# Kernel tuning notes

Measured on AMD Instinct MI355X. Metric: run time of the kernel, lower is better.

## Reference

```python
import jax, jax.numpy as jnp
import numpy as np
from jax import lax

# dims: B=2, C=dim=64, H=W=128 -> N=16384 tokens; d_inner=128, d_state=16, dt_rank=4, d_conv=4

def setup_inputs() -> dict:
    key = jax.random.key(0)
    ks = jax.random.split(key, 8)
    def n(k, shp, scale=0.02):
        return jax.random.normal(k, shp, jnp.float32) * scale
    d_inner, d_state, dt_rank = 128, 16, 4
    return {
        "x": jax.random.normal(ks[0], (2, 64, 128, 128), jnp.float32),
        "ln_w": jnp.ones((64,), jnp.float32),
        "ln_b": jnp.zeros((64,), jnp.float32),
        "in_proj_w": n(ks[1], (2 * d_inner, 64)),
        "conv_w": n(ks[2], (d_inner, 1, 4), 0.1),
        "conv_b": jnp.zeros((d_inner,), jnp.float32),
        "x_proj_w": n(ks[3], (dt_rank + 2 * d_state, d_inner)),
        "dt_proj_w": n(ks[4], (d_inner, dt_rank), 0.5),
        "dt_proj_b": n(ks[5], (d_inner,), 0.1),
        "A_log": jnp.log(jnp.broadcast_to(jnp.arange(1, d_state + 1, dtype=jnp.float32), (d_inner, d_state))),
        "D_param": jnp.ones((d_inner,), jnp.float32),
        "out_proj_w": n(ks[6], (64, d_inner)),
        "out_proj_b": jnp.zeros((64,), jnp.float32),
    }


def reference(x, ln_w, ln_b, in_proj_w, conv_w, conv_b, x_proj_w,
              dt_proj_w, dt_proj_b, A_log, D_param, out_proj_w, out_proj_b):
    B, C, H, W = x.shape
    d_inner = in_proj_w.shape[0] // 2
    d_state = A_log.shape[1]
    dt_rank = dt_proj_w.shape[1]
    eps = 1e-5

    # feature2token + channel LayerNorm (Restormer WithBias LN over C)
    t = x.reshape(B, C, H * W).transpose(0, 2, 1)  # [B, N, C]
    mu = jnp.mean(t, axis=-1, keepdims=True)
    var = jnp.var(t, axis=-1, keepdims=True)
    t = (t - mu) * lax.rsqrt(var + eps) * ln_w + ln_b

    # in_proj -> x, z
    xz = jnp.einsum('bnc,dc->bnd', t, in_proj_w)  # [B, N, 2*d_inner]
    x_in, z = jnp.split(xz, 2, axis=-1)

    # depthwise causal conv1d (k=4, pad left 3), then SiLU
    u = lax.conv_general_dilated(
        x_in.transpose(0, 2, 1), conv_w,
        window_strides=(1,), padding=[(3, 0)],
        feature_group_count=d_inner,
        dimension_numbers=('NCH', 'OIH', 'NCH'))
    u = jax.nn.silu(u + conv_b[None, :, None]).transpose(0, 2, 1)  # [B, N, d_inner]

    # x_proj -> dt, B, C of the SSM
    x_dbl = jnp.einsum('bnd,ed->bne', u, x_proj_w)
    dt_r = x_dbl[..., :dt_rank]
    Bmat = x_dbl[..., dt_rank:dt_rank + d_state]   # [B, N, d_state]
    Cmat = x_dbl[..., dt_rank + d_state:]          # [B, N, d_state]
    dt = jax.nn.softplus(jnp.einsum('bnr,dr->bnd', dt_r, dt_proj_w) + dt_proj_b)

    # selective scan: h_t = exp(dt*A) h_{t-1} + dt*B*u
    A = -jnp.exp(A_log)  # [d_inner, d_state]
    deltaA = jnp.exp(jnp.einsum('bnd,ds->bnds', dt, A))
    deltaBu = jnp.einsum('bnd,bns,bnd->bnds', dt, Bmat, u)

    def combine(c1, c2):
        a1, b1 = c1
        a2, b2 = c2
        return a2 * a1, a2 * b1 + b2

    _, h = lax.associative_scan(combine, (deltaA, deltaBu), axis=1)  # h: [B, N, d_inner, d_state]

    y = jnp.einsum('bnds,bns->bnd', h, Cmat) + u * D_param
    y = y * jax.nn.silu(z)
    out = jnp.einsum('bnd,cd->bnc', y, out_proj_w) + out_proj_b  # [B, N, C]

    # token2feature
    return out.transpose(0, 2, 1).reshape(B, C, H, W)
```

## Files before the change

### kernel.cpp

```cpp
#include <hip/hip_runtime.h>
#include <math.h>

#define NTOK 16384
#define DIN  128
#define NCH  512
#define CHL  32
#define NG   32
#define GCH  16

__device__ __forceinline__ float silu_f(float x)    { return x / (1.f + __expf(-x)); }
__device__ __forceinline__ float softplus_f(float x){ return (x > 20.f) ? x : log1pf(__expf(x)); }

__global__ __launch_bounds__(256) void k12(
    const float* __restrict__ x, const float* __restrict__ lnw,
    const float* __restrict__ lnb, const float* __restrict__ Win,
    const float* __restrict__ cw, const float* __restrict__ cb,
    float* __restrict__ zbuf, float* __restrict__ u)
{
  __shared__ __align__(16) float bufA[128*69];
  __shared__ __align__(16) float bufB[67*68];
  __shared__ float ps[256], pq[256];
  __shared__ float mu[67], rs[67];

  int t = threadIdx.x;
  int b  = blockIdx.x >> 8;
  int n0 = (blockIdx.x & 255) << 6;
  const float* xb = x + (size_t)b*64*NTOK;

  int tok = t & 63, quad = t >> 6;
  float s0 = 0.f, s1 = 0.f;
  for (int i = 0; i < 16; ++i) {
    int c = i*4 + quad;
    float v = xb[(size_t)c*NTOK + n0 + tok];
    bufA[c*68 + tok + 3] = v;
    s0 += v; s1 += v*v;
  }
  ps[t] = s0; pq[t] = s1;
  float vh = 0.f;
  if (t < 192) {
    int c = t & 63, k = t >> 6;
    int n = n0 - 3 + k;
    vh = (n >= 0) ? xb[(size_t)c*NTOK + n] : 0.f;
    bufA[c*68 + k] = vh;
  }
  __syncthreads();
  if (t < 192) {
    float a0 = vh, a1 = vh*vh;
    #pragma unroll
    for (int m = 1; m < 64; m <<= 1) { a0 += __shfl_xor(a0, m); a1 += __shfl_xor(a1, m); }
    if ((t & 63) == 0) {
      int k = t >> 6;
      float m = a0 * 0.015625f;
      float q = a1 * 0.015625f - m*m;
      mu[k] = m; rs[k] = rsqrtf(q + 1e-5f);
    }
  }
  if (t < 64) {
    float m = ps[t] + ps[64+t] + ps[128+t] + ps[192+t];
    float q = pq[t] + pq[64+t] + pq[128+t] + pq[192+t];
    m *= 0.015625f;
    q = q*0.015625f - m*m;
    mu[t+3] = m; rs[t+3] = rsqrtf(q + 1e-5f);
  }
  __syncthreads();
  {
    int c = t & 63, tq = t >> 6;
    float wv = lnw[c], bv = lnb[c];
    #pragma unroll
    for (int i = 0; i < 17; ++i) {
      int tp = tq + 4*i;
      if (tp < 67) {
        float val = (tp < 3 && n0 == 0) ? 0.f
                  : (bufA[c*68 + tp] - mu[tp]) * rs[tp] * wv + bv;
        bufB[tp*68 + c] = val;
      }
    }
  }

  int tokg = t & 15, dg = t >> 4;
  const float4* TB = (const float4*)bufB;

  __syncthreads();
  for (int i = 0; i < 32; ++i) {
    int idx = i*256 + t;
    int c = idx & 63, dd = idx >> 6;
    bufA[dd*68 + c] = Win[(128 + dd)*64 + c];
  }
  __syncthreads();
  {
    const float4* WA = (const float4*)bufA;
    float acc[4][8];
    #pragma unroll
    for (int i = 0; i < 4; ++i)
      #pragma unroll
      for (int j = 0; j < 8; ++j) acc[i][j] = 0.f;
    #pragma unroll 4
    for (int c4 = 0; c4 < 16; ++c4) {
      float4 tv[4], wv[8];
      #pragma unroll
      for (int i = 0; i < 4; ++i) tv[i] = TB[(3 + tokg + 16*i)*17 + c4];
      #pragma unroll
      for (int j = 0; j < 8; ++j) wv[j] = WA[(dg + 16*j)*17 + c4];
      #pragma unroll
      for (int i = 0; i < 4; ++i)
        #pragma unroll
        for (int j = 0; j < 8; ++j)
          acc[i][j] += tv[i].x*wv[j].x + tv[i].y*wv[j].y
                     + tv[i].z*wv[j].z + tv[i].w*wv[j].w;
    }
    #pragma unroll
    for (int i = 0; i < 4; ++i) {
      long n = (long)b*NTOK + n0 + tokg + 16*i;
      #pragma unroll
      for (int j = 0; j < 8; ++j)
        zbuf[n*128 + dg + 16*j] = silu_f(acc[i][j]);
    }
  }

  __syncthreads();
  for (int i = 0; i < 32; ++i) {
    int idx = i*256 + t;
    int c = idx & 63, dd = idx >> 6;
    bufA[dd*68 + c] = Win[dd*64 + c];
  }
  __syncthreads();
  float acc[4][8], acch[8];
  {
    const float4* WA = (const float4*)bufA;
    #pragma unroll
    for (int i = 0; i < 4; ++i)
      #pragma unroll
      for (int j = 0; j < 8; ++j) acc[i][j] = 0.f;
    #pragma unroll
    for (int j = 0; j < 8; ++j) acch[j] = 0.f;
    #pragma unroll 4
    for (int c4 = 0; c4 < 16; ++c4) {
      float4 tv[4], wv[8];
      #pragma unroll
      for (int i = 0; i < 4; ++i) tv[i] = TB[(3 + tokg + 16*i)*17 + c4];
      #pragma unroll
      for (int j = 0; j < 8; ++j) wv[j] = WA[(dg + 16*j)*17 + c4];
      #pragma unroll
      for (int i = 0; i < 4; ++i)
        #pragma unroll
        for (int j = 0; j < 8; ++j)
          acc[i][j] += tv[i].x*wv[j].x + tv[i].y*wv[j].y
                     + tv[i].z*wv[j].z + tv[i].w*wv[j].w;
      if (tokg < 3) {
        float4 th = TB[tokg*17 + c4];
        #pragma unroll
        for (int j = 0; j < 8; ++j)
          acch[j] += th.x*wv[j].x + th.y*wv[j].y + th.z*wv[j].z + th.w*wv[j].w;
      }
    }
  }
  __syncthreads();
  #pragma unroll
  for (int i = 0; i < 4; ++i)
    #pragma unroll
    for (int j = 0; j < 8; ++j)
      bufA[(dg + 16*j)*69 + 3 + tokg + 16*i] = acc[i][j];
  if (tokg < 3)
    #pragma unroll
    for (int j = 0; j < 8; ++j)
      bufA[(dg + 16*j)*69 + tokg] = acch[j];
  __syncthreads();

  {
    int d = t & 127, th = t >> 7;
    float w0 = cw[d*4], w1 = cw[d*4+1], w2 = cw[d*4+2], w3 = cw[d*4+3];
    float cbv = cb[d];
    int base = d*69 + th*32;
    float xa = bufA[base], xb2 = bufA[base+1], xc = bufA[base+2];
    long g0 = (long)b*NTOK + n0 + th*32;
    #pragma unroll
    for (int j = 0; j < 32; ++j) {
      float xd = bufA[base + j + 3];
      u[(g0 + j)*128 + d] = silu_f(w0*xa + w1*xb2 + w2*xc + w3*xd + cbv);
      xa = xb2; xb2 = xc; xc = xd;
    }
  }
}

__global__ __launch_bounds__(256) void k3_xproj_dt(
    const float* __restrict__ u, const float* __restrict__ Wx,
    const float* __restrict__ Wdt, const float* __restrict__ db,
    float* __restrict__ dt, float* __restrict__ Bm, float* __restrict__ Cm)
{
  __shared__ __align__(16) float wx[36*128];
  __shared__ float wdtT[4*128];
  __shared__ __align__(16) float xdbl[64*40];
  int t = threadIdx.x;
  for (int i = t; i < 1152; i += 256)
    *(float4*)&wx[i*4] = *(const float4*)&Wx[i*4];
  for (int i = t; i < 512; i += 256)
    wdtT[(i&3)*128 + (i>>2)] = Wdt[i];
  __syncthreads();

  long tok0 = (long)blockIdx.x * 64;
  int tok = t & 63, grp = t >> 6;
  const float* urow = u + (tok0 + tok)*128;

  float acc[9];
  #pragma unroll
  for (int e = 0; e < 9; ++e) acc[e] = 0.f;
  #pragma unroll 8
  for (int d4 = 0; d4 < 32; ++d4) {
    float4 uv = *(const float4*)&urow[d4*4];
    #pragma unroll
    for (int e = 0; e < 9; ++e) {
      float4 wv = *(const float4*)&wx[(grp*9+e)*128 + d4*4];
      acc[e] += uv.x*wv.x + uv.y*wv.y + uv.z*wv.z + uv.w*wv.w;
    }
  }
  #pragma unroll
  for (int e = 0; e < 9; ++e) xdbl[tok*40 + grp*9 + e] = acc[e];
  __syncthreads();

  {
    int tk = t >> 2, q = t & 3;
    float4 bv = *(const float4*)&xdbl[tk*40 + 4  + q*4];
    float4 cv = *(const float4*)&xdbl[tk*40 + 20 + q*4];
    *(float4*)&Bm[(tok0+tk)*16 + q*4] = bv;
    *(float4*)&Cm[(tok0+tk)*16 + q*4] = cv;
  }
  int d = t & 127, th = t >> 7;
  float w0 = wdtT[d], w1 = wdtT[128+d], w2 = wdtT[256+d], w3 = wdtT[384+d];
  float bias = db[d];
  for (int j = 0; j < 32; ++j) {
    int tk = th*32 + j;
    float a = bias + xdbl[tk*40]*w0 + xdbl[tk*40+1]*w1
                   + xdbl[tk*40+2]*w2 + xdbl[tk*40+3]*w3;
    dt[(tok0+tk)*128 + d] = softplus_f(a);
  }
}

__global__ __launch_bounds__(128) void k4a_local(
    const float* __restrict__ dt, const float* __restrict__ u,
    const float* __restrict__ Bm, const float* __restrict__ Alog,
    float* __restrict__ carP, float* __restrict__ carH)
{
  int d = threadIdx.x;
  int b = blockIdx.x / NCH, ch = blockIdx.x % NCH;
  long nb = (long)b*NTOK + (long)ch*CHL;
  float A[16], h[16], P[16];
  #pragma unroll
  for (int k = 0; k < 4; ++k) {
    float4 a = *(const float4*)&Alog[d*16 + k*4];
    A[k*4+0] = -__expf(a.x); A[k*4+1] = -__expf(a.y);
    A[k*4+2] = -__expf(a.z); A[k*4+3] = -__expf(a.w);
  }
  #pragma unroll
  for (int s = 0; s < 16; ++s) { h[s] = 0.f; P[s] = 1.f; }
  for (int i = 0; i < CHL; ++i) {
    long n = nb + i;
    float dtv = dt[n*128 + d];
    float uv  = u [n*128 + d];
    float du  = dtv * uv;
    float Bv[16];
    #pragma unroll
    for (int k = 0; k < 4; ++k) {
      float4 v = *(const float4*)&Bm[n*16 + k*4];
      Bv[k*4]=v.x; Bv[k*4+1]=v.y; Bv[k*4+2]=v.z; Bv[k*4+3]=v.w;
    }
    #pragma unroll
    for (int s = 0; s < 16; ++s) {
      float dA = __expf(dtv * A[s]);
      h[s] = dA*h[s] + du*Bv[s];
      P[s] *= dA;
    }
  }
  long cbs = ((long)(b*NCH + ch)*128 + d) * 16;
  #pragma unroll
  for (int k = 0; k < 4; ++k) {
    *(float4*)&carP[cbs + k*4] = make_float4(P[k*4],P[k*4+1],P[k*4+2],P[k*4+3]);
    *(float4*)&carH[cbs + k*4] = make_float4(h[k*4],h[k*4+1],h[k*4+2],h[k*4+3]);
  }
}

__global__ __launch_bounds__(256) void k4b1_group(
    float* __restrict__ cP, float* __restrict__ cH,
    float* __restrict__ Pg, float* __restrict__ Hg)
{
  int idx = blockIdx.x*256 + threadIdx.x;
  int rem = idx & 2047;
  int g   = (idx >> 11) & (NG-1);
  int b   = idx >> 16;
  float P = 1.f, H = 0.f;
  long base = ((long)b*NCH + g*GCH)*2048 + rem;
  #pragma unroll 4
  for (int j = 0; j < GCH; ++j) {
    long a = base + (long)j*2048;
    float p = cP[a], h = cH[a];
    cP[a] = P; cH[a] = H;
    H = p*H + h;
    P = p*P;
  }
  long ga = ((long)b*NG + g)*2048 + rem;
  Pg[ga] = P; Hg[ga] = H;
}

__global__ __launch_bounds__(256) void k4b2_carry(
    const float* __restrict__ Pg, float* __restrict__ Hg)
{
  int idx = blockIdx.x*256 + threadIdx.x;
  int b = idx >> 11, rem = idx & 2047;
  float H = 0.f;
  #pragma unroll 4
  for (int g = 0; g < NG; ++g) {
    long a = ((long)b*NG + g)*2048 + rem;
    float p = Pg[a], h = Hg[a];
    Hg[a] = H;
    H = p*H + h;
  }
}

__global__ __launch_bounds__(128) void k46(
    const float* __restrict__ dt, const float* __restrict__ u,
    const float* __restrict__ Bm, const float* __restrict__ Cm,
    const float* __restrict__ Alog, const float* __restrict__ Dp,
    const float* __restrict__ zs, const float* __restrict__ pPre,
    const float* __restrict__ hPre, const float* __restrict__ Hg,
    const float* __restrict__ Wout, const float* __restrict__ ob,
    float* __restrict__ out)
{
  __shared__ __align__(16) float yl[32*132];
  __shared__ __align__(16) float wo[64*128];
  int t = threadIdx.x;
  for (int i = 0; i < 16; ++i) {
    int idx = i*128 + t;
    *(float4*)&wo[idx*4] = *(const float4*)&Wout[idx*4];
  }

  int d = t;
  int b = blockIdx.x / NCH, ch = blockIdx.x % NCH;
  long nb = (long)b*NTOK + (long)ch*CHL;
  float A[16], h[16];
  #pragma unroll
  for (int k = 0; k < 4; ++k) {
    float4 a = *(const float4*)&Alog[d*16 + k*4];
    A[k*4+0] = -__expf(a.x); A[k*4+1] = -__expf(a.y);
    A[k*4+2] = -__expf(a.z); A[k*4+3] = -__expf(a.w);
  }
  long cbs = ((long)(b*NCH + ch)*128 + d) * 16;
  long gbs = ((long)b*NG + (ch >> 4))*2048 + d*16;
  #pragma unroll
  for (int k = 0; k < 4; ++k) {
    float4 hp = *(const float4*)&hPre[cbs + k*4];
    float4 pp = *(const float4*)&pPre[cbs + k*4];
    float4 gi = *(const float4*)&Hg[gbs + k*4];
    h[k*4+0] = hp.x + pp.x*gi.x; h[k*4+1] = hp.y + pp.y*gi.y;
    h[k*4+2] = hp.z + pp.z*gi.z; h[k*4+3] = hp.w + pp.w*gi.w;
  }
  float Dv = Dp[d];
  for (int i = 0; i < CHL; ++i) {
    long n = nb + i;
    float dtv = dt[n*128 + d];
    float uv  = u [n*128 + d];
    float du  = dtv * uv;
    float Bv[16], Cv[16];
    #pragma unroll
    for (int k = 0; k < 4; ++k) {
      float4 v = *(const float4*)&Bm[n*16 + k*4];
      Bv[k*4]=v.x; Bv[k*4+1]=v.y; Bv[k*4+2]=v.z; Bv[k*4+3]=v.w;
      float4 w = *(const float4*)&Cm[n*16 + k*4];
      Cv[k*4]=w.x; Cv[k*4+1]=w.y; Cv[k*4+2]=w.z; Cv[k*4+3]=w.w;
    }
    float y = 0.f;
    #pragma unroll
    for (int s = 0; s < 16; ++s) {
      float dA = __expf(dtv * A[s]);
      h[s] = dA*h[s] + du*Bv[s];
      y += h[s]*Cv[s];
    }
    yl[i*132 + d] = (y + uv*Dv) * zs[n*128 + d];
  }
  __syncthreads();

  {
    int tok = t & 31, cg = t >> 5;
    float acc[16];
    #pragma unroll
    for (int cc = 0; cc < 16; ++cc) acc[cc] = 0.f;
    #pragma unroll 4
    for (int d4 = 0; d4 < 32; ++d4) {
      float4 yv = *(const float4*)&yl[tok*132 + d4*4];
      #pragma unroll
      for (int cc = 0; cc < 16; ++cc) {
        float4 wv = *(const float4*)&wo[(cg*16+cc)*128 + d4*4];
        acc[cc] += yv.x*wv.x + yv.y*wv.y + yv.z*wv.z + yv.w*wv.w;
      }
    }
    long col = (long)ch*CHL + tok;
    #pragma unroll
    for (int cc = 0; cc < 16; ++cc) {
      int c = cg*16 + cc;
      out[((long)b*64 + c)*NTOK + col] = acc[cc] + ob[c];
    }
  }
}

extern "C" void kernel_launch(void* const* d_in, const int* in_sizes, int n_in,
                              void* d_out, int out_size, void* d_ws, size_t ws_size,
                              hipStream_t stream)
{
  (void)in_sizes; (void)n_in; (void)out_size; (void)ws_size;
  const float* x    = (const float*)d_in[0];
  const float* lnw  = (const float*)d_in[1];
  const float* lnb  = (const float*)d_in[2];
  const float* Win  = (const float*)d_in[3];
  const float* cw   = (const float*)d_in[4];
  const float* cb   = (const float*)d_in[5];
  const float* Wx   = (const float*)d_in[6];
  const float* Wdt  = (const float*)d_in[7];
  const float* db   = (const float*)d_in[8];
  const float* Alog = (const float*)d_in[9];
  const float* Dp   = (const float*)d_in[10];
  const float* Wout = (const float*)d_in[11];
  const float* ob   = (const float*)d_in[12];
  float* out = (float*)d_out;

  float* w   = (float*)d_ws;
  float* z   = w;
  float* u   = w + 4194304;
  float* dt  = w + 8388608;
  float* Bm  = w + 12582912;
  float* Cm  = w + 13107200;
  float* cP  = w + 13631488;
  float* cH  = w + 15728640;
  float* Pg  = w + 17825792;
  float* Hg  = w + 17956864;

  k12        <<<512, 256, 0, stream>>>(x, lnw, lnb, Win, cw, cb, z, u);
  k3_xproj_dt<<<512, 256, 0, stream>>>(u, Wx, Wdt, db, dt, Bm, Cm);
  k4a_local  <<<1024,128, 0, stream>>>(dt, u, Bm, Alog, cP, cH);
  k4b1_group <<<512, 256, 0, stream>>>(cP, cH, Pg, Hg);
  k4b2_carry <<<16,  256, 0, stream>>>(Pg, Hg);
  k46        <<<1024,128, 0, stream>>>(dt, u, Bm, Cm, Alog, Dp, z, cP, cH, Hg,
                                       Wout, ob, out);
}
```

Baseline: 182.7 us.

## Split scan state across thread pairs and separate out-projection into own kernel

The local scan and apply kernels now use two threads per channel, each handling 8 of the 16 state entries. The partial y values are combined with a warp shuffle. This doubles the number of threads per block and halves per-thread register pressure and serial work. The fused out-projection is moved into a new kernel that reads y*silu(z) from a workspace buffer and computes a register-tiled 32-token by 64-channel GEMM, at the cost of an extra global round trip for y and one more launch.

```diff
diff --git a/kernel.cpp b/kernel.cpp
--- a/kernel.cpp
+++ b/kernel.cpp
@@ -235,44 +235,45 @@
   }
 }
 
-__global__ __launch_bounds__(128) void k4a_local(
+__global__ __launch_bounds__(256) void k4a_local(
     const float* __restrict__ dt, const float* __restrict__ u,
     const float* __restrict__ Bm, const float* __restrict__ Alog,
     float* __restrict__ carP, float* __restrict__ carH)
 {
-  int d = threadIdx.x;
+  int t = threadIdx.x;
+  int d = t >> 1, sh = t & 1;
   int b = blockIdx.x / NCH, ch = blockIdx.x % NCH;
   long nb = (long)b*NTOK + (long)ch*CHL;
-  float A[16], h[16], P[16];
-  #pragma unroll
-  for (int k = 0; k < 4; ++k) {
-    float4 a = *(const float4*)&Alog[d*16 + k*4];
+  float A[8], h[8], P[8];
+  #pragma unroll
+  for (int k = 0; k < 2; ++k) {
+    float4 a = *(const float4*)&Alog[d*16 + sh*8 + k*4];
     A[k*4+0] = -__expf(a.x); A[k*4+1] = -__expf(a.y);
     A[k*4+2] = -__expf(a.z); A[k*4+3] = -__expf(a.w);
   }
   #pragma unroll
-  for (int s = 0; s < 16; ++s) { h[s] = 0.f; P[s] = 1.f; }
+  for (int s = 0; s < 8; ++s) { h[s] = 0.f; P[s] = 1.f; }
   for (int i = 0; i < CHL; ++i) {
     long n = nb + i;
     float dtv = dt[n*128 + d];
     float uv  = u [n*128 + d];
     float du  = dtv * uv;
-    float Bv[16];
-    #pragma unroll
-    for (int k = 0; k < 4; ++k) {
-      float4 v = *(const float4*)&Bm[n*16 + k*4];
+    float Bv[8];
+    #pragma unroll
+    for (int k = 0; k < 2; ++k) {
+      float4 v = *(const float4*)&Bm[n*16 + sh*8 + k*4];
       Bv[k*4]=v.x; Bv[k*4+1]=v.y; Bv[k*4+2]=v.z; Bv[k*4+3]=v.w;
     }
     #pragma unroll
-    for (int s = 0; s < 16; ++s) {
+    for (int s = 0; s < 8; ++s) {
       float dA = __expf(dtv * A[s]);
       h[s] = dA*h[s] + du*Bv[s];
       P[s] *= dA;
     }
   }
-  long cbs = ((long)(b*NCH + ch)*128 + d) * 16;
-  #pragma unroll
-  for (int k = 0; k < 4; ++k) {
+  long cbs = ((long)(b*NCH + ch)*128 + d)*16 + sh*8;
+  #pragma unroll
+  for (int k = 0; k < 2; ++k) {
     *(float4*)&carP[cbs + k*4] = make_float4(P[k*4],P[k*4+1],P[k*4+2],P[k*4+3]);
     *(float4*)&carH[cbs + k*4] = make_float4(h[k*4],h[k*4+1],h[k*4+2],h[k*4+3]);
   }
@@ -315,37 +316,29 @@
   }
 }
 
-__global__ __launch_bounds__(128) void k46(
+__global__ __launch_bounds__(256) void k4c_apply(
     const float* __restrict__ dt, const float* __restrict__ u,
     const float* __restrict__ Bm, const float* __restrict__ Cm,
     const float* __restrict__ Alog, const float* __restrict__ Dp,
     const float* __restrict__ zs, const float* __restrict__ pPre,
     const float* __restrict__ hPre, const float* __restrict__ Hg,
-    const float* __restrict__ Wout, const float* __restrict__ ob,
-    float* __restrict__ out)
-{
-  __shared__ __align__(16) float yl[32*132];
-  __shared__ __align__(16) float wo[64*128];
+    float* __restrict__ yz)
+{
   int t = threadIdx.x;
-  for (int i = 0; i < 16; ++i) {
-    int idx = i*128 + t;
-    *(float4*)&wo[idx*4] = *(const float4*)&Wout[idx*4];
-  }
-
-  int d = t;
+  int d = t >> 1, sh = t & 1;
   int b = blockIdx.x / NCH, ch = blockIdx.x % NCH;
   long nb = (long)b*NTOK + (long)ch*CHL;
-  float A[16], h[16];
-  #pragma unroll
-  for (int k = 0; k < 4; ++k) {
-    float4 a = *(const float4*)&Alog[d*16 + k*4];
+  float A[8], h[8];
+  #pragma unroll
+  for (int k = 0; k < 2; ++k) {
+    float4 a = *(const float4*)&Alog[d*16 + sh*8 + k*4];
     A[k*4+0] = -__expf(a.x); A[k*4+1] = -__expf(a.y);
     A[k*4+2] = -__expf(a.z); A[k*4+3] = -__expf(a.w);
   }
-  long cbs = ((long)(b*NCH + ch)*128 + d) * 16;
-  long gbs = ((long)b*NG + (ch >> 4))*2048 + d*16;
-  #pragma unroll
-  for (int k = 0; k < 4; ++k) {
+  long cbs = ((long)(b*NCH + ch)*128 + d)*16 + sh*8;
+  long gbs = ((long)b*NG + (ch >> 4))*2048 + d*16 + sh*8;
+  #pragma unroll
+  for (int k = 0; k < 2; ++k) {
     float4 hp = *(const float4*)&hPre[cbs + k*4];
     float4 pp = *(const float4*)&pPre[cbs + k*4];
     float4 gi = *(const float4*)&Hg[gbs + k*4];
@@ -358,45 +351,65 @@
     float dtv = dt[n*128 + d];
     float uv  = u [n*128 + d];
     float du  = dtv * uv;
-    float Bv[16], Cv[16];
-    #pragma unroll
-    for (int k = 0; k < 4; ++k) {
-      float4 v = *(const float4*)&Bm[n*16 + k*4];
+    float Bv[8], Cv[8];
+    #pragma unroll
+    for (int k = 0; k < 2; ++k) {
+      float4 v = *(const float4*)&Bm[n*16 + sh*8 + k*4];
       Bv[k*4]=v.x; Bv[k*4+1]=v.y; Bv[k*4+2]=v.z; Bv[k*4+3]=v.w;
-      float4 w = *(const float4*)&Cm[n*16 + k*4];
+      float4 w = *(const float4*)&Cm[n*16 + sh*8 + k*4];
       Cv[k*4]=w.x; Cv[k*4+1]=w.y; Cv[k*4+2]=w.z; Cv[k*4+3]=w.w;
     }
     float y = 0.f;
     #pragma unroll
-    for (int s = 0; s < 16; ++s) {
+    for (int s = 0; s < 8; ++s) {
       float dA = __expf(dtv * A[s]);
       h[s] = dA*h[s] + du*Bv[s];
       y += h[s]*Cv[s];
     }
-    yl[i*132 + d] = (y + uv*Dv) * zs[n*128 + d];
-  }
-  __syncthreads();
-
-  {
-    int tok = t & 31, cg = t >> 5;
-    float acc[16];
-    #pragma unroll
-    for (int cc = 0; cc < 16; ++cc) acc[cc] = 0.f;
-    #pragma unroll 4
-    for (int d4 = 0; d4 < 32; ++d4) {
-      float4 yv = *(const float4*)&yl[tok*132 + d4*4];
-      #pragma unroll
-      for (int cc = 0; cc < 16; ++cc) {
-        float4 wv = *(const float4*)&wo[(cg*16+cc)*128 + d4*4];
-        acc[cc] += yv.x*wv.x + yv.y*wv.y + yv.z*wv.z + yv.w*wv.w;
-      }
-    }
-    long col = (long)ch*CHL + tok;
-    #pragma unroll
-    for (int cc = 0; cc < 16; ++cc) {
-      int c = cg*16 + cc;
-      out[((long)b*64 + c)*NTOK + col] = acc[cc] + ob[c];
-    }
+    y += __shfl_xor(y, 1);
+    if (sh == 0)
+      yz[n*128 + d] = (y + uv*Dv) * zs[n*128 + d];
+  }
+}
+
+__global__ __launch_bounds__(256) void k6_outproj(
+    const float* __restrict__ yz, const float* __restrict__ Wout,
+    const float* __restrict__ ob, float* __restrict__ out)
+{
+  __shared__ __align__(16) float wo[64*132];
+  __shared__ __align__(16) float yl[32*132];
+  int t = threadIdx.x;
+  long tok0 = (long)blockIdx.x * 32;
+  for (int i = 0; i < 8; ++i) {
+    int g = i*256 + t; int c = g >> 5, q = g & 31;
+    *(float4*)&wo[c*132 + q*4] = *(const float4*)&Wout[c*128 + q*4];
+  }
+  for (int i = 0; i < 4; ++i) {
+    int g = i*256 + t; int tok = g >> 5, q = g & 31;
+    *(float4*)&yl[tok*132 + q*4] = *(const float4*)&yz[(tok0 + tok)*128 + q*4];
+  }
+  __syncthreads();
+  int tp = t & 15;
+  int tg = t >> 4;
+  float acc[4][2] = {{0.f}};
+  for (int d4 = 0; d4 < 32; ++d4) {
+    float4 y0 = *(const float4*)&yl[tg*132 + d4*4];
+    float4 y1 = *(const float4*)&yl[(tg+16)*132 + d4*4];
+    #pragma unroll
+    for (int cc = 0; cc < 4; ++cc) {
+      float4 wv = *(const float4*)&wo[(tp + 16*cc)*132 + d4*4];
+      acc[cc][0] += wv.x*y0.x + wv.y*y0.y + wv.z*y0.z + wv.w*y0.w;
+      acc[cc][1] += wv.x*y1.x + wv.y*y1.y + wv.z*y1.z + wv.w*y1.w;
+    }
+  }
+  int b  = (int)(tok0 / NTOK);
+  long n0 = tok0 % NTOK;
+  #pragma unroll
+  for (int cc = 0; cc < 4; ++cc) {
+    int c = tp + 16*cc;
+    float bias = ob[c];
+    out[((long)b*64 + c)*NTOK + n0 + tg     ] = acc[cc][0] + bias;
+    out[((long)b*64 + c)*NTOK + n0 + tg + 16] = acc[cc][1] + bias;
   }
 }
 
@@ -430,12 +443,13 @@
   float* cH  = w + 15728640;
   float* Pg  = w + 17825792;
   float* Hg  = w + 17956864;
+  float* yz  = w + 18087936;
 
   k12        <<<512, 256, 0, stream>>>(x, lnw, lnb, Win, cw, cb, z, u);
   k3_xproj_dt<<<512, 256, 0, stream>>>(u, Wx, Wdt, db, dt, Bm, Cm);
-  k4a_local  <<<1024,128, 0, stream>>>(dt, u, Bm, Alog, cP, cH);
+  k4a_local  <<<1024,256, 0, stream>>>(dt, u, Bm, Alog, cP, cH);
   k4b1_group <<<512, 256, 0, stream>>>(cP, cH, Pg, Hg);
   k4b2_carry <<<16,  256, 0, stream>>>(Pg, Hg);
-  k46        <<<1024,128, 0, stream>>>(dt, u, Bm, Cm, Alog, Dp, z, cP, cH, Hg,
-                                       Wout, ob, out);
-}
+  k4c_apply  <<<1024,256, 0, stream>>>(dt, u, Bm, Cm, Alog, Dp, z, cP, cH, Hg, yz);
+  k6_outproj <<<1024,256, 0, stream>>>(yz, Wout, ob, out);
+}
```

Result: faster. 164.3 us (-10.1%).
